# Optimization experiments

Hardware: AMD Instinct MI355X
Metric: run time of the kernel (lower is better)

The kernel has to match this reference:

```python
import jax, jax.numpy as jnp
import numpy as np

N_HEAD = 16

def setup_inputs() -> dict:
    key = jax.random.key(0)
    k1, k2, k3 = jax.random.split(key, 3)
    C = 2048
    x = jax.random.normal(k1, (2, 2048, C), dtype=jnp.float32)
    w_attn = jax.random.normal(k2, (3 * C, C), dtype=jnp.float32) * (1.0 / np.sqrt(C))
    w_proj = jax.random.normal(k3, (C, C), dtype=jnp.float32) * (1.0 / np.sqrt(C))
    return {"x": x, "w_attn": w_attn, "w_proj": w_proj}

def reference(x, w_attn, w_proj):
    B, T, C = x.shape
    H = N_HEAD
    hd = C // H
    # fused QKV projection (torch Linear: x @ W.T)
    qkv = jnp.einsum('btc,fc->btf', x, w_attn)          # [B, T, 3C]
    q, k, v = jnp.split(qkv, 3, axis=2)
    q = q.reshape(B, T, H, hd).transpose(0, 2, 1, 3)     # [B, H, T, hd]
    k = k.reshape(B, T, H, hd).transpose(0, 2, 1, 3)
    v = v.reshape(B, T, H, hd).transpose(0, 2, 1, 3)
    scale = 1.0 / jnp.sqrt(jnp.asarray(hd, dtype=x.dtype))
    scores = jnp.einsum('bhqd,bhkd->bhqk', q, k) * scale  # [B, H, T, T]
    causal = jnp.tril(jnp.ones((T, T), dtype=bool))
    scores = jnp.where(causal, scores, jnp.finfo(scores.dtype).min)
    attn = jax.nn.softmax(scores, axis=-1)
    y = jnp.einsum('bhqk,bhkd->bhqd', attn, v)           # [B, H, T, hd]
    y = y.transpose(0, 2, 1, 3).reshape(B, T, C)
    return jnp.einsum('btc,oc->bto', y, w_proj)
```

## Files before the change

### kernel.cpp

```cpp
#include <hip/hip_runtime.h>
#include <stdint.h>
#include <stddef.h>

#define B_   2
#define T_   2048
#define C_   2048
#define H_   16
#define HD_  128
#define M_   4096
#define N1_  6144
#define NQK_ 4096

typedef __attribute__((ext_vector_type(8))) short short8;
typedef __attribute__((ext_vector_type(4))) float float4v;
typedef __attribute__((ext_vector_type(4))) unsigned short ushort4v;
typedef __attribute__((ext_vector_type(8))) unsigned short ushort8v;

#define QSCALE_ (0.088388347648318447f * 1.4426950408889634f)

static __device__ __forceinline__ unsigned short f32_to_bf16(float f) {
    union { float f; unsigned u; } v; v.f = f;
    unsigned r = v.u + 0x7FFFu + ((v.u >> 16) & 1u);
    return (unsigned short)(r >> 16);
}

static __device__ __forceinline__ void load16(const unsigned short* g, unsigned short* l) {
    __builtin_amdgcn_global_load_lds(
        (const __attribute__((address_space(1))) unsigned int*)g,
        (__attribute__((address_space(3))) unsigned int*)l, 16, 0, 0);
}

__global__ void cvt_bf16_kernel(const float* __restrict__ src,
                                unsigned short* __restrict__ dst, int n) {
    int i = (blockIdx.x * blockDim.x + threadIdx.x) * 8;
    if (i >= n) return;
    float4v a = *(const float4v*)(src + i);
    float4v c = *(const float4v*)(src + i + 4);
    ushort8v o;
    o[0] = f32_to_bf16(a[0]); o[1] = f32_to_bf16(a[1]);
    o[2] = f32_to_bf16(a[2]); o[3] = f32_to_bf16(a[3]);
    o[4] = f32_to_bf16(c[0]); o[5] = f32_to_bf16(c[1]);
    o[6] = f32_to_bf16(c[2]); o[7] = f32_to_bf16(c[3]);
    *(ushort8v*)(dst + i) = o;
}

template<int MODE>
__global__ __launch_bounds__(256, 4) void gemm_bt_kernel(
    const unsigned short* __restrict__ A,
    const unsigned short* __restrict__ Bt,
    unsigned short* __restrict__ out_qk,
    unsigned short* __restrict__ out_vt,
    float* __restrict__ out_f,
    int Kdim, int Ndim_out)
{
    __shared__ unsigned short lds_a[128 * 32];
    __shared__ unsigned short lds_b[128 * 32];

    const int t = threadIdx.x;
    const int bm = blockIdx.x * 128;
    const int bn = blockIdx.y * 128;
    const int wave = t >> 6, lane = t & 63;
    const int wr = (wave >> 1) * 64, wc = (wave & 1) * 64;
    const int fr = lane & 15, quad = lane >> 4;

    const int srow = t >> 2, skc = (t & 3) * 8;
    const unsigned short* ga0 = A + (size_t)(bm + srow) * Kdim + skc;
    const unsigned short* ga1 = ga0 + (size_t)64 * Kdim;
    const unsigned short* gb0 = Bt + (size_t)(bn + srow) * Kdim + skc;
    const unsigned short* gb1 = gb0 + (size_t)64 * Kdim;
    unsigned short* la0 = lds_a + t * 8;
    unsigned short* la1 = lds_a + (t + 256) * 8;
    unsigned short* lb0 = lds_b + t * 8;
    unsigned short* lb1 = lds_b + (t + 256) * 8;

    float4v acc[4][4];
#pragma unroll
    for (int i = 0; i < 4; ++i)
#pragma unroll
        for (int j = 0; j < 4; ++j) acc[i][j] = (float4v){0.f, 0.f, 0.f, 0.f};

    for (int k0 = 0; k0 < Kdim; k0 += 32) {
        __syncthreads();
        load16(ga0 + k0, la0);
        load16(ga1 + k0, la1);
        load16(gb0 + k0, lb0);
        load16(gb1 + k0, lb1);
        __syncthreads();

        short8 af[4], bfr[4];
#pragma unroll
        for (int i = 0; i < 4; ++i)
            af[i] = *(const short8*)(lds_a + (wr + i * 16 + fr) * 32 + quad * 8);
#pragma unroll
        for (int j = 0; j < 4; ++j)
            bfr[j] = *(const short8*)(lds_b + (wc + j * 16 + fr) * 32 + quad * 8);
#pragma unroll
        for (int i = 0; i < 4; ++i)
#pragma unroll
            for (int j = 0; j < 4; ++j)
                acc[i][j] = __builtin_amdgcn_mfma_f32_16x16x32_bf16(af[i], bfr[j], acc[i][j], 0, 0, 0);
    }

    if (MODE == 0) {
        if (bn < NQK_) {
            const float qs = (bn < C_) ? QSCALE_ : 1.0f;
#pragma unroll
            for (int i = 0; i < 4; ++i) {
                int m0 = bm + wr + i * 16 + quad * 4;
#pragma unroll
                for (int j = 0; j < 4; ++j) {
                    int col = bn + wc + j * 16 + fr;
#pragma unroll
                    for (int r = 0; r < 4; ++r)
                        out_qk[(size_t)(m0 + r) * NQK_ + col] = f32_to_bf16(acc[i][j][r] * qs);
                }
            }
        } else {
#pragma unroll
            for (int i = 0; i < 4; ++i) {
                int m0 = bm + wr + i * 16 + quad * 4;
                int bb = m0 >> 11, tt = m0 & (T_ - 1);
#pragma unroll
                for (int j = 0; j < 4; ++j) {
                    int fcol = (bn - NQK_) + wc + j * 16 + fr;
                    int hh = fcol >> 7, dd = fcol & 127;
                    ushort4v pk;
                    pk[0] = f32_to_bf16(acc[i][j][0]);
                    pk[1] = f32_to_bf16(acc[i][j][1]);
                    pk[2] = f32_to_bf16(acc[i][j][2]);
                    pk[3] = f32_to_bf16(acc[i][j][3]);
                    *(ushort4v*)(out_vt + ((size_t)((bb * H_ + hh) * HD_ + dd)) * T_ + tt) = pk;
                }
            }
        }
    } else {
#pragma unroll
        for (int i = 0; i < 4; ++i) {
            int m0 = bm + wr + i * 16 + quad * 4;
#pragma unroll
            for (int j = 0; j < 4; ++j) {
                int col = bn + wc + j * 16 + fr;
#pragma unroll
                for (int r = 0; r < 4; ++r)
                    out_f[(size_t)(m0 + r) * Ndim_out + col] = acc[i][j][r];
            }
        }
    }
}

__global__ __launch_bounds__(512, 4) void attn_kernel(
    const unsigned short* __restrict__ qk,
    const unsigned short* __restrict__ vtg,
    unsigned short* __restrict__ y)
{
    __shared__ unsigned short kt[64 * 128];
    __shared__ unsigned short vtile[128 * 64];
    __shared__ unsigned short pt[8][16 * 72];

    const int t = threadIdx.x;
    const int wave = t >> 6, lane = t & 63;
    const int fr = lane & 15, quad = lane >> 4;

    const int idx = blockIdx.x;
    const int b  = idx >> 8;
    const int h  = (idx >> 4) & 15;
    const int q4 = idx & 15;
    const int qt = b ? q4 : (15 - q4);
    const int q0 = qt * 128;
    const int wq = q0 + wave * 16;

    short8 qf[4];
    {
        const unsigned short* qp = qk + (size_t)(b * T_ + wq + fr) * NQK_ + h * HD_ + quad * 8;
#pragma unroll
        for (int kk = 0; kk < 4; ++kk)
            qf[kk] = *(const short8*)(qp + kk * 32);
    }

    float lrow[4];
    float4v oacc[8];
#pragma unroll
    for (int r = 0; r < 4; ++r) lrow[r] = 0.f;
#pragma unroll
    for (int dj = 0; dj < 8; ++dj) oacc[dj] = (float4v){0.f, 0.f, 0.f, 0.f};

    const int nkt = (q0 >> 6) + 2;
    const unsigned short* kbase_g = qk + (size_t)(b * T_) * NQK_ + C_ + h * HD_;
    const unsigned short* vbase_g = vtg + (size_t)((b * H_ + h) * HD_) * T_;

    for (int kti = 0; kti < nkt; ++kti) {
        const int k0 = kti * 64;
        __syncthreads();
#pragma unroll
        for (int rr = 0; rr < 2; ++rr) {
            int c = t + rr * 512;
            int kkey = c >> 4;
            int kd = ((c & 15) ^ (kkey & 15)) * 8;
            load16(kbase_g + (size_t)(k0 + kkey) * NQK_ + kd, kt + c * 8);
            int vd = c >> 3;
            int vk = ((c & 7) ^ (vd & 7)) * 8;
            load16(vbase_g + (size_t)vd * T_ + k0 + vk, vtile + c * 8);
        }
        __syncthreads();

        if (k0 > wq + 15) continue;

        float4v s[4];
#pragma unroll
        for (int j = 0; j < 4; ++j) s[j] = (float4v){0.f, 0.f, 0.f, 0.f};
#pragma unroll
        for (int kk = 0; kk < 4; ++kk) {
            short8 kf[4];
#pragma unroll
            for (int j = 0; j < 4; ++j)
                kf[j] = *(const short8*)(kt + ((j * 16 + fr) * 16 + ((kk * 4 + quad) ^ fr)) * 8);
#pragma unroll
            for (int j = 0; j < 4; ++j)
                s[j] = __builtin_amdgcn_mfma_f32_16x16x32_bf16(qf[kk], kf[j], s[j], 0, 0, 0);
        }

        const bool need_mask = (k0 + 63 > wq);
#pragma unroll
        for (int r = 0; r < 4; ++r) {
            const int qrow = wq + quad * 4 + r;
#pragma unroll
            for (int j = 0; j < 4; ++j) {
                float p = exp2f(s[j][r]);
                if (need_mask && (k0 + j * 16 + fr > qrow)) p = 0.f;
                s[j][r] = p;
                lrow[r] += p;
            }
        }

        unsigned short* pw = pt[wave];
#pragma unroll
        for (int j = 0; j < 4; ++j)
#pragma unroll
            for (int r = 0; r < 4; ++r)
                pw[(quad * 4 + r) * 72 + j * 16 + fr] = f32_to_bf16(s[j][r]);

#pragma unroll
        for (int kk2 = 0; kk2 < 2; ++kk2) {
            short8 pf = *(const short8*)(pw + fr * 72 + kk2 * 32 + quad * 8);
#pragma unroll
            for (int dj = 0; dj < 8; ++dj) {
                short8 vf = *(const short8*)(vtile + ((dj * 16 + fr) * 8 + ((kk2 * 4 + quad) ^ (fr & 7))) * 8);
                oacc[dj] = __builtin_amdgcn_mfma_f32_16x16x32_bf16(pf, vf, oacc[dj], 0, 0, 0);
            }
        }
    }

#pragma unroll
    for (int r = 0; r < 4; ++r) {
        float sum = lrow[r];
        sum += __shfl_xor(sum, 1);
        sum += __shfl_xor(sum, 2);
        sum += __shfl_xor(sum, 4);
        sum += __shfl_xor(sum, 8);
        float inv = 1.0f / sum;
        int m = b * T_ + wq + quad * 4 + r;
#pragma unroll
        for (int dj = 0; dj < 8; ++dj)
            y[(size_t)m * C_ + h * HD_ + dj * 16 + fr] = f32_to_bf16(oacc[dj][r] * inv);
    }
}

extern "C" void kernel_launch(void* const* d_in, const int* in_sizes, int n_in,
                              void* d_out, int out_size, void* d_ws, size_t ws_size,
                              hipStream_t stream) {
    (void)in_sizes; (void)n_in; (void)out_size; (void)ws_size;
    const float* x      = (const float*)d_in[0];
    const float* w_attn = (const float*)d_in[1];
    const float* w_proj = (const float*)d_in[2];
    float* out = (float*)d_out;

    char* ws = (char*)d_ws;
    unsigned short* xb  = (unsigned short*)(ws);
    unsigned short* wab = (unsigned short*)(ws + 16777216);
    unsigned short* wpb = (unsigned short*)(ws + 41943040);
    unsigned short* qkb = (unsigned short*)(ws + 50331648);
    unsigned short* vtb = (unsigned short*)(ws + 83886080);
    unsigned short* yb  = (unsigned short*)(ws + 100663296);

    cvt_bf16_kernel<<<(M_ * C_ / 8 + 255) / 256, 256, 0, stream>>>(x, xb, M_ * C_);
    cvt_bf16_kernel<<<(N1_ * C_ / 8 + 255) / 256, 256, 0, stream>>>(w_attn, wab, N1_ * C_);
    cvt_bf16_kernel<<<(C_ * C_ / 8 + 255) / 256, 256, 0, stream>>>(w_proj, wpb, C_ * C_);

    gemm_bt_kernel<0><<<dim3(M_ / 128, N1_ / 128), 256, 0, stream>>>(
        xb, wab, qkb, vtb, nullptr, C_, 0);

    attn_kernel<<<B_ * H_ * (T_ / 128), 512, 0, stream>>>(qkb, vtb, yb);

    gemm_bt_kernel<1><<<dim3(M_ / 128, C_ / 128), 256, 0, stream>>>(
        yb, wpb, nullptr, nullptr, out, C_, C_);
}
```

Baseline: 377.5 us.

## Merge conversion kernels, deepen GEMM K-tile with swizzle, shrink attention blocks

The three fp32-to-bf16 conversion launches become a single kernel that picks its source by block index. The GEMM K-step doubles to 64 and uses an XOR-swizzled LDS layout, halving barrier count and reducing bank conflicts on fragment reads. The attention kernel moves from 128-query blocks of 8 waves to 64-query blocks of 4 waves, with a new causal load-balancing order across blocks. Together these target launch overhead, GEMM synchronisation and LDS conflicts, and causal tail imbalance, at the cost of more LDS per GEMM block and more K/V tile reloads in attention.

```diff
diff --git a/kernel.cpp b/kernel.cpp
--- a/kernel.cpp
+++ b/kernel.cpp
@@ -30,18 +30,23 @@
         (__attribute__((address_space(3))) unsigned int*)l, 16, 0, 0);
 }
 
-__global__ void cvt_bf16_kernel(const float* __restrict__ src,
-                                unsigned short* __restrict__ dst, int n) {
-    int i = (blockIdx.x * blockDim.x + threadIdx.x) * 8;
-    if (i >= n) return;
-    float4v a = *(const float4v*)(src + i);
-    float4v c = *(const float4v*)(src + i + 4);
+__global__ void cvt3_kernel(const float* __restrict__ sx, unsigned short* __restrict__ dx,
+                            const float* __restrict__ sa, unsigned short* __restrict__ da,
+                            const float* __restrict__ sp, unsigned short* __restrict__ dp) {
+    int blk = blockIdx.x;
+    const float* s; unsigned short* d; int base;
+    if (blk < 4096)      { s = sx; d = dx; base = blk * 2048; }
+    else if (blk < 10240){ s = sa; d = da; base = (blk - 4096) * 2048; }
+    else                 { s = sp; d = dp; base = (blk - 10240) * 2048; }
+    int i = base + threadIdx.x * 8;
+    float4v a = *(const float4v*)(s + i);
+    float4v c = *(const float4v*)(s + i + 4);
     ushort8v o;
     o[0] = f32_to_bf16(a[0]); o[1] = f32_to_bf16(a[1]);
     o[2] = f32_to_bf16(a[2]); o[3] = f32_to_bf16(a[3]);
     o[4] = f32_to_bf16(c[0]); o[5] = f32_to_bf16(c[1]);
     o[6] = f32_to_bf16(c[2]); o[7] = f32_to_bf16(c[3]);
-    *(ushort8v*)(dst + i) = o;
+    *(ushort8v*)(d + i) = o;
 }
 
 template<int MODE>
@@ -53,8 +58,8 @@
     float* __restrict__ out_f,
     int Kdim, int Ndim_out)
 {
-    __shared__ unsigned short lds_a[128 * 32];
-    __shared__ unsigned short lds_b[128 * 32];
+    __shared__ unsigned short lds_a[128 * 64];
+    __shared__ unsigned short lds_b[128 * 64];
 
     const int t = threadIdx.x;
     const int bm = blockIdx.x * 128;
@@ -63,15 +68,10 @@
     const int wr = (wave >> 1) * 64, wc = (wave & 1) * 64;
     const int fr = lane & 15, quad = lane >> 4;
 
-    const int srow = t >> 2, skc = (t & 3) * 8;
-    const unsigned short* ga0 = A + (size_t)(bm + srow) * Kdim + skc;
-    const unsigned short* ga1 = ga0 + (size_t)64 * Kdim;
-    const unsigned short* gb0 = Bt + (size_t)(bn + srow) * Kdim + skc;
-    const unsigned short* gb1 = gb0 + (size_t)64 * Kdim;
-    unsigned short* la0 = lds_a + t * 8;
-    unsigned short* la1 = lds_a + (t + 256) * 8;
-    unsigned short* lb0 = lds_b + t * 8;
-    unsigned short* lb1 = lds_b + (t + 256) * 8;
+    const int srow0 = t >> 3;
+    const int scol  = ((t & 7) ^ (srow0 & 7)) * 8;
+    const unsigned short* ga = A + (size_t)(bm + srow0) * Kdim + scol;
+    const unsigned short* gb = Bt + (size_t)(bn + srow0) * Kdim + scol;
 
     float4v acc[4][4];
 #pragma unroll
@@ -79,26 +79,30 @@
 #pragma unroll
         for (int j = 0; j < 4; ++j) acc[i][j] = (float4v){0.f, 0.f, 0.f, 0.f};
 
-    for (int k0 = 0; k0 < Kdim; k0 += 32) {
-        __syncthreads();
-        load16(ga0 + k0, la0);
-        load16(ga1 + k0, la1);
-        load16(gb0 + k0, lb0);
-        load16(gb1 + k0, lb1);
-        __syncthreads();
-
-        short8 af[4], bfr[4];
-#pragma unroll
-        for (int i = 0; i < 4; ++i)
-            af[i] = *(const short8*)(lds_a + (wr + i * 16 + fr) * 32 + quad * 8);
-#pragma unroll
-        for (int j = 0; j < 4; ++j)
-            bfr[j] = *(const short8*)(lds_b + (wc + j * 16 + fr) * 32 + quad * 8);
-#pragma unroll
-        for (int i = 0; i < 4; ++i)
+    for (int k0 = 0; k0 < Kdim; k0 += 64) {
+        __syncthreads();
+#pragma unroll
+        for (int rr = 0; rr < 4; ++rr) {
+            load16(ga + (size_t)(32 * rr) * Kdim + k0, lds_a + (t + rr * 256) * 8);
+            load16(gb + (size_t)(32 * rr) * Kdim + k0, lds_b + (t + rr * 256) * 8);
+        }
+        __syncthreads();
+
+#pragma unroll
+        for (int k2 = 0; k2 < 2; ++k2) {
+            short8 af[4], bfr[4];
+#pragma unroll
+            for (int i = 0; i < 4; ++i)
+                af[i] = *(const short8*)(lds_a + ((wr + i * 16 + fr) * 8 + ((k2 * 4 + quad) ^ (fr & 7))) * 8);
 #pragma unroll
             for (int j = 0; j < 4; ++j)
-                acc[i][j] = __builtin_amdgcn_mfma_f32_16x16x32_bf16(af[i], bfr[j], acc[i][j], 0, 0, 0);
+                bfr[j] = *(const short8*)(lds_b + ((wc + j * 16 + fr) * 8 + ((k2 * 4 + quad) ^ (fr & 7))) * 8);
+#pragma unroll
+            for (int i = 0; i < 4; ++i)
+#pragma unroll
+                for (int j = 0; j < 4; ++j)
+                    acc[i][j] = __builtin_amdgcn_mfma_f32_16x16x32_bf16(af[i], bfr[j], acc[i][j], 0, 0, 0);
+        }
     }
 
     if (MODE == 0) {
@@ -148,25 +152,26 @@
     }
 }
 
-__global__ __launch_bounds__(512, 4) void attn_kernel(
+__global__ __launch_bounds__(256, 4) void attn_kernel(
     const unsigned short* __restrict__ qk,
     const unsigned short* __restrict__ vtg,
     unsigned short* __restrict__ y)
 {
     __shared__ unsigned short kt[64 * 128];
     __shared__ unsigned short vtile[128 * 64];
-    __shared__ unsigned short pt[8][16 * 72];
+    __shared__ unsigned short pt[4][16 * 72];
 
     const int t = threadIdx.x;
     const int wave = t >> 6, lane = t & 63;
     const int fr = lane & 15, quad = lane >> 4;
 
     const int idx = blockIdx.x;
-    const int b  = idx >> 8;
-    const int h  = (idx >> 4) & 15;
-    const int q4 = idx & 15;
-    const int qt = b ? q4 : (15 - q4);
-    const int q0 = qt * 128;
+    const int pos  = idx & 31;
+    const int rest = idx >> 5;
+    const int b = rest >> 4;
+    const int h = rest & 15;
+    const int qt = (rest & 1) ? (31 - pos) : pos;
+    const int q0 = qt * 64;
     const int wq = q0 + wave * 16;
 
     short8 qf[4];
@@ -184,7 +189,7 @@
 #pragma unroll
     for (int dj = 0; dj < 8; ++dj) oacc[dj] = (float4v){0.f, 0.f, 0.f, 0.f};
 
-    const int nkt = (q0 >> 6) + 2;
+    const int nkt = qt + 1;
     const unsigned short* kbase_g = qk + (size_t)(b * T_) * NQK_ + C_ + h * HD_;
     const unsigned short* vbase_g = vtg + (size_t)((b * H_ + h) * HD_) * T_;
 
@@ -192,8 +197,8 @@
         const int k0 = kti * 64;
         __syncthreads();
 #pragma unroll
-        for (int rr = 0; rr < 2; ++rr) {
-            int c = t + rr * 512;
+        for (int rr = 0; rr < 4; ++rr) {
+            int c = t + rr * 256;
             int kkey = c >> 4;
             int kd = ((c & 15) ^ (kkey & 15)) * 8;
             load16(kbase_g + (size_t)(k0 + kkey) * NQK_ + kd, kt + c * 8);
@@ -282,14 +287,12 @@
     unsigned short* vtb = (unsigned short*)(ws + 83886080);
     unsigned short* yb  = (unsigned short*)(ws + 100663296);
 
-    cvt_bf16_kernel<<<(M_ * C_ / 8 + 255) / 256, 256, 0, stream>>>(x, xb, M_ * C_);
-    cvt_bf16_kernel<<<(N1_ * C_ / 8 + 255) / 256, 256, 0, stream>>>(w_attn, wab, N1_ * C_);
-    cvt_bf16_kernel<<<(C_ * C_ / 8 + 255) / 256, 256, 0, stream>>>(w_proj, wpb, C_ * C_);
+    cvt3_kernel<<<12288, 256, 0, stream>>>(x, xb, w_attn, wab, w_proj, wpb);
 
     gemm_bt_kernel<0><<<dim3(M_ / 128, N1_ / 128), 256, 0, stream>>>(
         xb, wab, qkb, vtb, nullptr, C_, 0);
 
-    attn_kernel<<<B_ * H_ * (T_ / 128), 512, 0, stream>>>(qkb, vtb, yb);
+    attn_kernel<<<B_ * H_ * (T_ / 64), 256, 0, stream>>>(qkb, vtb, yb);
 
     gemm_bt_kernel<1><<<dim3(M_ / 128, C_ / 128), 256, 0, stream>>>(
         yb, wpb, nullptr, nullptr, out, C_, C_);
```

Result: no change. 384.8 us (+1.9%).
